# Performance work log

Measured on AMD Instinct MI355X. Metric: run time of the kernel, lower is better.

The kernel has to match this reference:

```python
import jax, jax.numpy as jnp
import numpy as np

P = 0.8
XINT_MAX = 0.125; ROT_MAX = 10.0
BRI_STD = 0.2; CON_STD = 0.2; HUE_MAX = 0.95; SAT_STD = 0.2; SHARP_STD = 1.0; NOISE_STD = 0.1

def _gate(key, B, p):
    k1, k2 = jax.random.split(key)
    bern = jax.random.randint(k1, (B,), 0, 2).astype(jnp.float32)
    u = jax.random.uniform(k2, ())
    return bern * p > u  # [B] bool, matches randint(0,2)*flag*p > random()

def _sel(m, new, old):
    return jnp.where(m[:, None, None, None], new, old)

def _warp(imgs, angle_deg, tx, ty, nearest=False):
    # inverse-affine resample: rotate by angle (deg, CCW) about center, then translate (tx,ty) px; zero fill
    B, C, H, W = imgs.shape
    th = jnp.deg2rad(jnp.asarray(angle_deg, jnp.float32))
    c, s = jnp.cos(th), jnp.sin(th)
    cy, cx = (H - 1) / 2.0, (W - 1) / 2.0
    ys, xs = jnp.meshgrid(jnp.arange(H, dtype=jnp.float32), jnp.arange(W, dtype=jnp.float32), indexing='ij')
    dx = xs - cx - tx; dy = ys - cy - ty
    sx = c * dx + s * dy + cx
    sy = -s * dx + c * dy + cy
    if nearest:
        xi = jnp.round(sx); yi = jnp.round(sy)
        valid = (xi >= 0) & (xi < W) & (yi >= 0) & (yi < H)
        xc = jnp.clip(xi, 0, W - 1).astype(jnp.int32)
        yc = jnp.clip(yi, 0, H - 1).astype(jnp.int32)
        return imgs[:, :, yc, xc] * valid
    x0 = jnp.floor(sx); y0 = jnp.floor(sy)
    wx = sx - x0; wy = sy - y0
    def g(yi, xi):
        valid = (xi >= 0) & (xi < W) & (yi >= 0) & (yi < H)
        yc = jnp.clip(yi, 0, H - 1).astype(jnp.int32)
        xc = jnp.clip(xi, 0, W - 1).astype(jnp.int32)
        return imgs[:, :, yc, xc] * valid
    v00 = g(y0, x0); v01 = g(y0, x0 + 1); v10 = g(y0 + 1, x0); v11 = g(y0 + 1, x0 + 1)
    top = v00 * (1 - wx) + v01 * wx
    bot = v10 * (1 - wx) + v11 * wx
    return top * (1 - wy) + bot * wy

def _gray(x):
    return 0.2989 * x[:, 0:1] + 0.587 * x[:, 1:2] + 0.114 * x[:, 2:3]

def _blend(a, b, ratio):
    return jnp.clip(ratio * a + (1.0 - ratio) * b, 0.0, 1.0)

def _rgb_to_hsv(x):
    r, g, b = x[:, 0], x[:, 1], x[:, 2]
    maxc = jnp.maximum(jnp.maximum(r, g), b)
    minc = jnp.minimum(jnp.minimum(r, g), b)
    cr = maxc - minc
    s = cr / jnp.where(maxc == 0, 1.0, maxc)
    crd = jnp.where(cr == 0, 1.0, cr)
    rc = (maxc - r) / crd; gc = (maxc - g) / crd; bc = (maxc - b) / crd
    h = jnp.where(maxc == r, bc - gc, jnp.where(maxc == g, 2.0 + rc - bc, 4.0 + gc - rc))
    h = jnp.where(cr == 0, 0.0, (h / 6.0) % 1.0)
    return jnp.stack([h, s, maxc], axis=1)

def _hsv_to_rgb(x):
    h, s, v = x[:, 0], x[:, 1], x[:, 2]
    i = jnp.floor(h * 6.0)
    f = h * 6.0 - i
    p = v * (1 - s); q = v * (1 - f * s); t = v * (1 - (1 - f) * s)
    ii = i.astype(jnp.int32) % 6
    conds = [ii == 0, ii == 1, ii == 2, ii == 3, ii == 4, ii == 5]
    r = jnp.select(conds, [v, q, p, p, t, v])
    g = jnp.select(conds, [t, v, v, q, p, p])
    b = jnp.select(conds, [p, p, t, v, v, q])
    return jnp.stack([r, g, b], axis=1)

def _sharp_degenerate(x):
    C, H, W = x.shape[1], x.shape[2], x.shape[3]
    k = jnp.array([[1., 1., 1.], [1., 5., 1.], [1., 1., 1.]], jnp.float32) / 13.0
    w = jnp.tile(k[None, None], (C, 1, 1, 1))
    blur = jax.lax.conv_general_dilated(x, w, (1, 1), 'SAME', feature_group_count=C,
                                        dimension_numbers=('NCHW', 'OIHW', 'NCHW'))
    blur = jnp.clip(blur, 0.0, 1.0)
    interior = jnp.zeros((H, W), bool).at[1:-1, 1:-1].set(True)
    return jnp.where(interior, blur, x)  # torchvision keeps original border pixels

def _augment(images, masks):
    key = jax.random.key(42)
    ks = jax.random.split(key, 18)
    B = images.shape[0]
    img = (images + 1.0) * 0.5
    msk = masks
    # xflip
    m = _gate(ks[0], B, P)
    img = _sel(m, img[:, :, :, ::-1], img)
    msk = _sel(m, msk[:, :, :, ::-1], msk)
    # rotate90 (square images: exact)
    m = _gate(ks[1], B, P)
    img = _sel(m, jnp.rot90(img, 1, axes=(2, 3)), img)
    msk = _sel(m, jnp.rot90(msk, 1, axes=(2, 3)), msk)
    # xint translation
    m = _gate(ks[2], B, P)
    t = jax.random.uniform(ks[3], ()) * XINT_MAX
    img = _sel(m, _warp(img, 0.0, t, t), img)
    msk = _sel(m, _warp(msk, 0.0, t, t, nearest=True), msk)
    # rotate
    m = _gate(ks[4], B, P)
    r = jax.random.uniform(ks[5], ()) * ROT_MAX
    img = _sel(m, _warp(img, r, 0.0, 0.0), img)
    msk = _sel(m, _warp(msk, r, 0.0, 0.0, nearest=True), msk)
    # hue
    m = _gate(ks[6], B, P)
    h = (jax.random.uniform(ks[7], ()) - 0.5) * HUE_MAX
    hsv = _rgb_to_hsv(jnp.clip(img, 0.0, 1.0))
    hsv = hsv.at[:, 0].set((hsv[:, 0] + h) % 1.0)
    img = _sel(m, _hsv_to_rgb(hsv), img)
    # brightness
    m = _gate(ks[8], B, P)
    b = jnp.abs(1.0 + jax.random.normal(ks[9], ()) * BRI_STD)
    img = _sel(m, jnp.clip(img * b, 0.0, 1.0), img)
    # contrast
    m = _gate(ks[10], B, P)
    c = jnp.abs(1.0 + jax.random.normal(ks[11], ()) * CON_STD)
    mean = _gray(img).mean(axis=(2, 3), keepdims=True)
    img = _sel(m, _blend(img, mean, c), img)
    # saturation
    m = _gate(ks[12], B, P)
    s = jnp.abs(1.0 + jax.random.normal(ks[13], ()) * SAT_STD)
    img = _sel(m, _blend(img, _gray(img), s), img)
    # sharpness (bug-faithful: std == self.sharpness == 1.0)
    m = _gate(ks[14], B, P)
    sh = jnp.abs(1.0 + jax.random.normal(ks[15], ()) * SHARP_STD)
    img = _sel(m, _blend(img, _sharp_degenerate(img), sh), img)
    # noise
    m = _gate(ks[16], B, P)
    n = jax.random.normal(ks[17], img.shape, img.dtype) * NOISE_STD
    img = _sel(m, img + n, img)
    img = (img - 0.5) / 0.5
    return img, msk

def setup_inputs() -> dict:
    key = jax.random.key(0)
    k1, k2 = jax.random.split(key)
    images = jax.random.uniform(k1, (32, 3, 512, 512), jnp.float32, -1.0, 1.0)
    masks = (jax.random.uniform(k2, (32, 1, 512, 512), jnp.float32) > 0.5).astype(jnp.float32)
    return {"images": images, "masks": masks}

def reference(images, masks):
    return _augment(images, masks)
```

## Files before the change

kernel.cpp:

```cpp
#include <hip/hip_runtime.h>
#include <stdint.h>
#include <math.h>

#define HH 512
#define WW 512
#define BB 32
#define CC 3
#define HWSZ (HH*WW)
#define CHW (CC*HWSZ)
#define NIMG (BB*CHW)
#define NMSK (BB*HWSZ)

__host__ __device__ inline uint32_t rotl32(uint32_t x, uint32_t r){ return (x<<r)|(x>>(32u-r)); }

__host__ __device__ inline void tf2x32(uint32_t k0, uint32_t k1, uint32_t x0, uint32_t x1,
                                       uint32_t& o0, uint32_t& o1){
  uint32_t kx = k0 ^ k1 ^ 0x1BD11BDAu;
  uint32_t ks[3] = {k0, k1, kx};
  const uint32_t R[2][4] = {{13u,15u,26u,6u},{17u,29u,16u,24u}};
  x0 += ks[0]; x1 += ks[1];
  #pragma unroll
  for (int i = 0; i < 5; ++i){
    #pragma unroll
    for (int j = 0; j < 4; ++j){
      x0 += x1; x1 = rotl32(x1, R[i & 1][j]); x1 ^= x0;
    }
    x0 += ks[(i+1)%3];
    x1 += ks[(i+2)%3] + (uint32_t)(i+1);
  }
  o0 = x0; o1 = x1;
}

__host__ __device__ inline float bits_to_u01(uint32_t b){
  uint32_t fb = (b >> 9) | 0x3f800000u;
  float f;
#ifdef __HIP_DEVICE_COMPILE__
  f = __uint_as_float(fb);
#else
  union { uint32_t u; float f; } cv; cv.u = fb; f = cv.f;
#endif
  return f - 1.0f;
}

__host__ __device__ inline float erfinv_f32(float x){
  float w = -log1pf(-x*x);
  float p;
  if (w < 5.0f){
    w -= 2.5f;
    p = 2.81022636e-08f;
    p = fmaf(p, w, 3.43273939e-07f);
    p = fmaf(p, w, -3.5233877e-06f);
    p = fmaf(p, w, -4.39150654e-06f);
    p = fmaf(p, w, 0.00021858087f);
    p = fmaf(p, w, -0.00125372503f);
    p = fmaf(p, w, -0.00417768164f);
    p = fmaf(p, w, 0.246640727f);
    p = fmaf(p, w, 1.50140941f);
  } else {
    w = sqrtf(w) - 3.0f;
    p = -0.000200214257f;
    p = fmaf(p, w, 0.000100950558f);
    p = fmaf(p, w, 0.00134934322f);
    p = fmaf(p, w, -0.00367342844f);
    p = fmaf(p, w, 0.00573950773f);
    p = fmaf(p, w, -0.0076224613f);
    p = fmaf(p, w, 0.00943887047f);
    p = fmaf(p, w, 1.00167406f);
    p = fmaf(p, w, 2.83297682f);
  }
  return p * x;
}

#define NRM_LO (-0.9999999403953552f)
#define SQRT2F 1.41421356237309504880f

__host__ __device__ inline float normal_from_bits(uint32_t b){
  float f = bits_to_u01(b);
  float val = f * 2.0f + NRM_LO;
  val = fmaxf(NRM_LO, val);
  return SQRT2F * erfinv_f32(val);
}

struct Key { uint32_t a, b; };

static Key foldSplit(Key k, uint32_t j){
  Key r; tf2x32(k.a, k.b, 0u, j, r.a, r.b); return r;
}

static uint32_t bits32(Key k, uint32_t i){
  uint32_t o0, o1; tf2x32(k.a, k.b, 0u, i, o0, o1); return o0 ^ o1;
}

static float unif_scalar(Key k){ return bits_to_u01(bits32(k, 0u)); }
static float normal_scalar(Key k){ return normal_from_bits(bits32(k, 0u)); }

static uint32_t gate_mask(Key kg){
  Key k1 = foldSplit(kg, 0u);
  Key k2 = foldSplit(kg, 1u);
  Key kl = foldSplit(k1, 1u);
  float u = bits_to_u01(bits32(k2, 0u));
  uint32_t m = 0;
  for (uint32_t i = 0; i < 32; ++i){
    float bern = (float)(bits32(kl, i) & 1u);
    if (bern * 0.8f > u) m |= (1u << i);
  }
  return m;
}

struct AugParams {
  uint32_t mFlip, mRot90, mTrans, mRot, mHue, mBri, mCon, mSat, mSharp, mNoise;
  float t, rotC, rotS, hShift, bri, con, sat, shp;
  uint32_t nk0, nk1;
};

__device__ inline float clip01(float v){ return fminf(fmaxf(v, 0.0f), 1.0f); }

__device__ inline void permIdx(int y, int x, bool r9, bool fl, int& py, int& px){
  if (r9){ py = x; px = 511 - y; } else { py = y; px = x; }
  if (fl) px = 511 - px;
}

__device__ inline float tapP(const float* __restrict__ src, int y, int x, bool r9, bool fl){
  if ((unsigned)x >= 512u || (unsigned)y >= 512u) return 0.0f;
  int py, px; permIdx(y, x, r9, fl, py, px);
  return (src[py*512 + px] + 1.0f) * 0.5f;
}

__device__ inline void stage1RGB(const float* __restrict__ base, int ty, int tx,
                                 bool r9, bool fl, bool tr, float t, float out[3]){
  if (!tr){
    #pragma unroll
    for (int c = 0; c < 3; ++c) out[c] = tapP(base + c*HWSZ, ty, tx, r9, fl);
    return;
  }
  float sx = (((float)tx - 255.5f) - t) + 255.5f;
  float sy = (((float)ty - 255.5f) - t) + 255.5f;
  float x0f = floorf(sx), y0f = floorf(sy);
  float wx = sx - x0f, wy = sy - y0f;
  int x0 = (int)x0f, y0 = (int)y0f;
  #pragma unroll
  for (int c = 0; c < 3; ++c){
    const float* s = base + c*HWSZ;
    float v00 = tapP(s, y0,   x0,   r9, fl);
    float v01 = tapP(s, y0,   x0+1, r9, fl);
    float v10 = tapP(s, y0+1, x0,   r9, fl);
    float v11 = tapP(s, y0+1, x0+1, r9, fl);
    float top = v00*(1.0f-wx) + v01*wx;
    float bot = v10*(1.0f-wx) + v11*wx;
    out[c] = top*(1.0f-wy) + bot*wy;
  }
}

__device__ inline void rotTap(const float* __restrict__ base, int ty, int tx,
                              bool r9, bool fl, bool tr, float t, float o[3]){
  if ((unsigned)tx < 512u && (unsigned)ty < 512u){
    stage1RGB(base, ty, tx, r9, fl, tr, t, o);
  } else {
    o[0] = o[1] = o[2] = 0.0f;
  }
}

__device__ inline void rgb2hsv(float r, float g, float b, float& h, float& s, float& v){
  float maxc = fmaxf(fmaxf(r, g), b);
  float minc = fminf(fminf(r, g), b);
  float cr = maxc - minc;
  s = cr / ((maxc == 0.0f) ? 1.0f : maxc);
  float crd = (cr == 0.0f) ? 1.0f : cr;
  float rc = (maxc - r) / crd;
  float gc = (maxc - g) / crd;
  float bc = (maxc - b) / crd;
  float hh;
  if (maxc == r)      hh = bc - gc;
  else if (maxc == g) hh = 2.0f + rc - bc;
  else                hh = 4.0f + gc - rc;
  if (cr == 0.0f) hh = 0.0f;
  else { hh = hh / 6.0f; hh = hh - floorf(hh); }
  h = hh; v = maxc;
}

__device__ inline void hsv2rgb(float h, float s, float v, float& r, float& g, float& b){
  float i = floorf(h * 6.0f);
  float f = h * 6.0f - i;
  float p = v * (1.0f - s);
  float q = v * (1.0f - f * s);
  float t = v * (1.0f - (1.0f - f) * s);
  int ii = ((int)i) % 6;
  switch (ii){
    case 0: r = v; g = t; b = p; break;
    case 1: r = q; g = v; b = p; break;
    case 2: r = p; g = v; b = t; break;
    case 3: r = p; g = q; b = v; break;
    case 4: r = t; g = p; b = v; break;
    default: r = v; g = p; b = q; break;
  }
}

__device__ inline void applyHB(float v[3], bool hue, bool bri, const AugParams& P){
  if (hue){
    float r = clip01(v[0]), g = clip01(v[1]), bb = clip01(v[2]);
    float h, s, val;
    rgb2hsv(r, g, bb, h, s, val);
    h = h + P.hShift;
    h = h - floorf(h);
    hsv2rgb(h, s, val, v[0], v[1], v[2]);
  }
  if (bri){
    #pragma unroll
    for (int c = 0; c < 3; ++c) v[c] = clip01(v[c] * P.bri);
  }
}

__device__ inline void stage2RGB(const float* __restrict__ base, int yy, int xx,
                                 const AugParams& P, int b, float v[3]){
  bool fl  = (P.mFlip  >> b) & 1u;
  bool r9  = (P.mRot90 >> b) & 1u;
  bool tr  = (P.mTrans >> b) & 1u;
  bool rot = (P.mRot   >> b) & 1u;
  if (rot){
    float dx = (float)xx - 255.5f;
    float dy = (float)yy - 255.5f;
    float sx = (P.rotC*dx + P.rotS*dy) + 255.5f;
    float sy = (-P.rotS*dx + P.rotC*dy) + 255.5f;
    float x0f = floorf(sx), y0f = floorf(sy);
    float wx = sx - x0f, wy = sy - y0f;
    int x0 = (int)x0f, y0 = (int)y0f;
    float q00[3], q01[3], q10[3], q11[3];
    rotTap(base, y0,   x0,   r9, fl, tr, P.t, q00);
    rotTap(base, y0,   x0+1, r9, fl, tr, P.t, q01);
    rotTap(base, y0+1, x0,   r9, fl, tr, P.t, q10);
    rotTap(base, y0+1, x0+1, r9, fl, tr, P.t, q11);
    #pragma unroll
    for (int c = 0; c < 3; ++c){
      float top = q00[c]*(1.0f-wx) + q01[c]*wx;
      float bot = q10[c]*(1.0f-wx) + q11[c]*wx;
      v[c] = top*(1.0f-wy) + bot*wy;
    }
  } else {
    stage1RGB(base, yy, xx, r9, fl, tr, P.t, v);
  }
  applyHB(v, (P.mHue >> b) & 1u, (P.mBri >> b) & 1u, P);
}

__device__ inline float s1at(const float* __restrict__ s, int y, int x){
  return ((unsigned)x < 512u && (unsigned)y < 512u) ? s[y*512 + x] : 0.0f;
}

__device__ inline void stage2S1(const float* __restrict__ s1b, int yy, int xx,
                                const AugParams& P, int b, float v[3]){
  bool rot = (P.mRot >> b) & 1u;
  bool hue = (P.mHue >> b) & 1u;
  bool bri = (P.mBri >> b) & 1u;
  if (rot){
    float dx = (float)xx - 255.5f;
    float dy = (float)yy - 255.5f;
    float sx = (P.rotC*dx + P.rotS*dy) + 255.5f;
    float sy = (-P.rotS*dx + P.rotC*dy) + 255.5f;
    float x0f = floorf(sx), y0f = floorf(sy);
    float wx = sx - x0f, wy = sy - y0f;
    int x0 = (int)x0f, y0 = (int)y0f;
    #pragma unroll
    for (int c = 0; c < 3; ++c){
      const float* s = s1b + c*HWSZ;
      float v00 = s1at(s, y0,   x0);
      float v01 = s1at(s, y0,   x0+1);
      float v10 = s1at(s, y0+1, x0);
      float v11 = s1at(s, y0+1, x0+1);
      float top = v00*(1.0f-wx) + v01*wx;
      float bot = v10*(1.0f-wx) + v11*wx;
      v[c] = top*(1.0f-wy) + bot*wy;
    }
  } else {
    #pragma unroll
    for (int c = 0; c < 3; ++c) v[c] = s1b[c*HWSZ + yy*512 + xx];
  }
  applyHB(v, hue, bri, P);
}

__device__ inline void procCS(float v[3], bool con, float cmul, float cadd, bool sat, float smul){
  if (con){
    #pragma unroll
    for (int c = 0; c < 3; ++c) v[c] = clip01(cmul * v[c] + cadd);
  }
  if (sat){
    float g = 0.2989f*v[0] + 0.587f*v[1] + 0.114f*v[2];
    float gadd = (1.0f - smul) * g;
    #pragma unroll
    for (int c = 0; c < 3; ++c) v[c] = clip01(smul * v[c] + gadd);
  }
}


__global__ void kZero(float* meanAcc){
  int t = threadIdx.x;
  if (t < 32) meanAcc[t] = 0.0f;
}


__global__ __launch_bounds__(256) void kStage1(const float* __restrict__ img,
                                               float* __restrict__ S1, AugParams P){
  __shared__ float ptile[33][33];
  int b = blockIdx.z;
  bool fl = (P.mFlip  >> b) & 1u;
  bool r9 = (P.mRot90 >> b) & 1u;
  bool tr = (P.mTrans >> b) & 1u;
  int X0 = blockIdx.x*32, Y0 = blockIdx.y*32;
  int tx = threadIdx.x, ty = threadIdx.y;
  int tid = ty*32 + tx;
  const float* base = img + (size_t)b*CHW;
  float t = P.t;

  if (!r9 && !tr){
    #pragma unroll
    for (int c = 0; c < 3; ++c){
      const float* src = base + c*HWSZ;
      float* dst = S1 + (size_t)b*CHW + (size_t)c*HWSZ;
      #pragma unroll
      for (int k = 0; k < 4; ++k){
        int y = Y0 + ty + 8*k;
        int x = X0 + tx;
        int px = fl ? (511 - x) : x;
        dst[(size_t)y*512 + x] = (src[y*512 + px] + 1.0f) * 0.5f;
      }
    }
    return;
  }

  for (int c = 0; c < 3; ++c){
    const float* src = base + c*HWSZ;
    for (int idx = tid; idx < 33*33; idx += 256){
      int r = idx / 33, q = idx - r*33;
      float val = 0.0f;
      if (!r9){
        int yy = Y0 - 1 + r;
        int xx = X0 - 1 + q;
        if ((unsigned)yy < 512u && (unsigned)xx < 512u){
          int px = fl ? (511 - xx) : xx;
          val = (src[yy*512 + px] + 1.0f) * 0.5f;
        }
        ptile[r][q] = val;
      } else {
        int xx = X0 - 1 + r;
        int yy = Y0 - 1 + q;
        if ((unsigned)yy < 512u && (unsigned)xx < 512u){
          int col = fl ? yy : (511 - yy);
          val = (src[xx*512 + col] + 1.0f) * 0.5f;
        }
        ptile[q][r] = val;
      }
    }
    __syncthreads();
    #pragma unroll
    for (int k = 0; k < 4; ++k){
      int y = Y0 + ty + 8*k;
      int x = X0 + tx;
      float o;
      if (tr){
        float sx = (((float)x - 255.5f) - t) + 255.5f;
        float sy = (((float)y - 255.5f) - t) + 255.5f;
        float x0f = floorf(sx), y0f = floorf(sy);
        float wx = sx - x0f, wy = sy - y0f;
        int lx0 = (int)x0f - (X0 - 1);
        int ly0 = (int)y0f - (Y0 - 1);
        float v00 = ptile[ly0][lx0],     v01 = ptile[ly0][lx0+1];
        float v10 = ptile[ly0+1][lx0],   v11 = ptile[ly0+1][lx0+1];
        float top = v00*(1.0f-wx) + v01*wx;
        float bot = v10*(1.0f-wx) + v11*wx;
        o = top*(1.0f-wy) + bot*wy;
      } else {
        o = ptile[ty + 8*k + 1][tx + 1];
      }
      S1[(size_t)b*CHW + (size_t)c*HWSZ + (size_t)y*512 + x] = o;
    }
    __syncthreads();
  }
}

__global__ __launch_bounds__(256) void kMaskStage(const float* __restrict__ msk,
                                                  float* __restrict__ M1,
                                                  float* __restrict__ outMsk, AugParams P){
  __shared__ float mtile[32][33];
  int b = blockIdx.z;
  bool fl  = (P.mFlip  >> b) & 1u;
  bool r9  = (P.mRot90 >> b) & 1u;
  bool rot = (P.mRot   >> b) & 1u;
  int X0 = blockIdx.x*32, Y0 = blockIdx.y*32;
  int tx = threadIdx.x, ty = threadIdx.y;
  int tid = ty*32 + tx;
  const float* src = msk + (size_t)b*HWSZ;
  float* dst = (rot ? M1 : outMsk) + (size_t)b*HWSZ;
  if (!r9){
    #pragma unroll
    for (int k = 0; k < 4; ++k){
      int y = Y0 + ty + 8*k, x = X0 + tx;
      int px = fl ? (511 - x) : x;
      dst[y*512 + x] = src[y*512 + px];
    }
  } else {
    for (int idx = tid; idx < 32*32; idx += 256){
      int r = idx >> 5, q = idx & 31;
      int xx = X0 + r;
      int yy = Y0 + q;
      int col = fl ? yy : (511 - yy);
      mtile[q][r] = src[xx*512 + col];
    }
    __syncthreads();
    #pragma unroll
    for (int k = 0; k < 4; ++k){
      int y = Y0 + ty + 8*k, x = X0 + tx;
      dst[y*512 + x] = mtile[ty + 8*k][tx];
    }
  }
}

__global__ __launch_bounds__(256) void kMaskRot(const float* __restrict__ M1,
                                                float* __restrict__ outMsk, AugParams P){
  int b = blockIdx.z;
  if (!((P.mRot >> b) & 1u)) return;
  int x = blockIdx.x*blockDim.x + threadIdx.x;
  int y = blockIdx.y*blockDim.y + threadIdx.y;
  float dx = __fsub_rn((float)x, 255.5f);
  float dy = __fsub_rn((float)y, 255.5f);
  float sx = __fadd_rn(__fadd_rn(__fmul_rn(P.rotC, dx), __fmul_rn(P.rotS, dy)), 255.5f);
  float sy = __fadd_rn(__fadd_rn(__fmul_rn(-P.rotS, dx), __fmul_rn(P.rotC, dy)), 255.5f);
  float xi = rintf(sx), yi = rintf(sy);
  bool valid = (xi >= 0.0f) && (xi < 512.0f) && (yi >= 0.0f) && (yi < 512.0f);
  int xc = (int)fminf(fmaxf(xi, 0.0f), 511.0f);
  int yc = (int)fminf(fmaxf(yi, 0.0f), 511.0f);
  float v = valid ? M1[(size_t)b*HWSZ + yc*512 + xc] : 0.0f;
  outMsk[(size_t)b*HWSZ + y*512 + x] = v;
}

__global__ __launch_bounds__(256) void kMean2(const float* __restrict__ S1,
                                              float* __restrict__ meanAcc, AugParams P){
  int b = blockIdx.z;
  if (!((P.mCon >> b) & 1u)) return;
  bool rot = (P.mRot >> b) & 1u;
  bool hue = (P.mHue >> b) & 1u;
  bool bri = (P.mBri >> b) & 1u;
  int tid = threadIdx.x;
  const float* base = S1 + (size_t)b*CHW;
  int pbase = blockIdx.x * 4096;
  float lsum = 0.0f;

  if (!rot){
    const float4* r4p = (const float4*)(base);
    const float4* g4p = (const float4*)(base + HWSZ);
    const float4* b4p = (const float4*)(base + 2*HWSZ);
    int q0 = (pbase >> 2) + tid;
    #pragma unroll
    for (int j = 0; j < 4; ++j){
      float4 r4 = r4p[q0 + j*256];
      float4 g4 = g4p[q0 + j*256];
      float4 b4 = b4p[q0 + j*256];
      float rr[4] = {r4.x, r4.y, r4.z, r4.w};
      float gg[4] = {g4.x, g4.y, g4.z, g4.w};
      float bb[4] = {b4.x, b4.y, b4.z, b4.w};
      #pragma unroll
      for (int e = 0; e < 4; ++e){
        float v[3] = {rr[e], gg[e], bb[e]};
        applyHB(v, hue, bri, P);
        lsum += 0.2989f*v[0] + 0.587f*v[1] + 0.114f*v[2];
      }
    }
  } else {
    #pragma unroll 4
    for (int j = 0; j < 16; ++j){
      int px = pbase + j*256 + tid;
      int y = px >> 9, x = px & 511;
      float v[3];
      stage2S1(base, y, x, P, b, v);
      lsum += 0.2989f*v[0] + 0.587f*v[1] + 0.114f*v[2];
    }
  }

  #pragma unroll
  for (int off = 32; off > 0; off >>= 1) lsum += __shfl_down(lsum, off);
  __shared__ float wsum[4];
  int wid = tid >> 6, lid = tid & 63;
  if (lid == 0) wsum[wid] = lsum;
  __syncthreads();
  if (tid == 0) atomicAdd(&meanAcc[b], wsum[0] + wsum[1] + wsum[2] + wsum[3]);
}

__global__ __launch_bounds__(256) void kFinal2(const float* __restrict__ S1,
                                               const float* __restrict__ meanAcc,
                                               float* __restrict__ out, AugParams P){
  __shared__ float s2[34][34][3];
  int tx = threadIdx.x, ty = threadIdx.y;
  int tid = ty*32 + tx;
  int bx = blockIdx.x, by = blockIdx.y, b = blockIdx.z;
  const float W1 = 1.0f/13.0f, W5 = 5.0f/13.0f;

  bool con = (P.mCon   >> b) & 1u;
  bool sat = (P.mSat   >> b) & 1u;
  bool shg = (P.mSharp >> b) & 1u;
  bool noi = (P.mNoise >> b) & 1u;
  float mean = meanAcc[b] * (1.0f/262144.0f);
  float cadd = (1.0f - P.con) * mean;
  const float* base = S1 + (size_t)b*CHW;

  for (int cell = tid; cell < 34*34; cell += 256){
    int r = cell / 34, cc = cell - r*34;
    int gy = by*32 + r - 1, gx = bx*32 + cc - 1;
    float v[3] = {0.0f, 0.0f, 0.0f};
    if ((unsigned)gx < 512u && (unsigned)gy < 512u){
      stage2S1(base, gy, gx, P, b, v);
      procCS(v, con, P.con, cadd, sat, P.sat);
    }
    s2[r][cc][0] = v[0]; s2[r][cc][1] = v[1]; s2[r][cc][2] = v[2];
  }
  __syncthreads();

  for (int k = 0; k < 4; ++k){
    int yy = ty + 8*k;
    int x = bx*32 + tx, y = by*32 + yy;
    bool interior = (x >= 1) && (x <= 510) && (y >= 1) && (y <= 510);
    float res[3];
    float c0[3] = { s2[yy+1][tx+1][0], s2[yy+1][tx+1][1], s2[yy+1][tx+1][2] };
    if (shg && interior){
      float nsum[3] = {0.0f, 0.0f, 0.0f};
      #pragma unroll
      for (int dy = 0; dy < 3; ++dy){
        #pragma unroll
        for (int dxx = 0; dxx < 3; ++dxx){
          if (dxx == 1 && dy == 1) continue;
          #pragma unroll
          for (int c = 0; c < 3; ++c) nsum[c] += s2[yy+dy][tx+dxx][c];
        }
      }
      #pragma unroll
      for (int c = 0; c < 3; ++c){
        float bl = clip01(nsum[c]*W1 + c0[c]*W5);
        res[c] = clip01(P.shp * c0[c] + (1.0f - P.shp) * bl);
      }
    } else {
      res[0] = c0[0]; res[1] = c0[1]; res[2] = c0[2];
    }

    if (noi){
      #pragma unroll
      for (int c = 0; c < 3; ++c){
        uint32_t idx = (uint32_t)(b*CHW + c*HWSZ + y*512 + x);
        uint32_t o0, o1;
        tf2x32(P.nk0, P.nk1, 0u, idx, o0, o1);
        res[c] += normal_from_bits(o0 ^ o1) * 0.1f;
      }
    }
    #pragma unroll
    for (int c = 0; c < 3; ++c){
      out[(size_t)b*CHW + (size_t)c*HWSZ + (size_t)y*512 + x] = (res[c] - 0.5f) * 2.0f;
    }
  }
}


__global__ __launch_bounds__(256) void kMask(const float* __restrict__ msk,
                                             float* __restrict__ out, AugParams P){
  int x = blockIdx.x*blockDim.x + threadIdx.x;
  int y = blockIdx.y*blockDim.y + threadIdx.y;
  int b = blockIdx.z;
  bool fl  = (P.mFlip  >> b) & 1u;
  bool r9  = (P.mRot90 >> b) & 1u;
  bool rot = (P.mRot   >> b) & 1u;
  float v;
  if (rot){
    float dx = __fsub_rn((float)x, 255.5f);
    float dy = __fsub_rn((float)y, 255.5f);
    float sx = __fadd_rn(__fadd_rn(__fmul_rn(P.rotC, dx), __fmul_rn(P.rotS, dy)), 255.5f);
    float sy = __fadd_rn(__fadd_rn(__fmul_rn(-P.rotS, dx), __fmul_rn(P.rotC, dy)), 255.5f);
    float xi = rintf(sx), yi = rintf(sy);
    bool valid = (xi >= 0.0f) && (xi < 512.0f) && (yi >= 0.0f) && (yi < 512.0f);
    int xc = (int)fminf(fmaxf(xi, 0.0f), 511.0f);
    int yc = (int)fminf(fmaxf(yi, 0.0f), 511.0f);
    int py, px; permIdx(yc, xc, r9, fl, py, px);
    v = valid ? msk[(size_t)b*HWSZ + py*512 + px] : 0.0f;
  } else {
    int py, px; permIdx(y, x, r9, fl, py, px);
    v = msk[(size_t)b*HWSZ + py*512 + px];
  }
  out[(size_t)b*HWSZ + y*512 + x] = v;
}

__global__ __launch_bounds__(256) void kMean(const float* __restrict__ img,
                                             float* __restrict__ meanAcc, AugParams P){
  int b = blockIdx.z;
  if (!((P.mCon >> b) & 1u)) return;
  int x = blockIdx.x*blockDim.x + threadIdx.x;
  int y = blockIdx.y*blockDim.y + threadIdx.y;
  float v[3];
  stage2RGB(img + (size_t)b*CHW, y, x, P, b, v);
  float gray = 0.2989f*v[0] + 0.587f*v[1] + 0.114f*v[2];
  __shared__ float sred[256];
  int tid = threadIdx.y*blockDim.x + threadIdx.x;
  sred[tid] = gray;
  __syncthreads();
  for (int s = 128; s > 0; s >>= 1){
    if (tid < s) sred[tid] += sred[tid + s];
    __syncthreads();
  }
  if (tid == 0) atomicAdd(&meanAcc[b], sred[0]);
}

__global__ __launch_bounds__(256) void kFinal(const float* __restrict__ img,
                                              const float* __restrict__ meanAcc,
                                              float* __restrict__ out, AugParams P){
  __shared__ float s2[10][34][3];
  int tx = threadIdx.x, ty = threadIdx.y;
  int tid = ty*32 + tx;
  int bx = blockIdx.x, by = blockIdx.y, b = blockIdx.z;
  const float W1 = 1.0f/13.0f, W5 = 5.0f/13.0f;

  bool con = (P.mCon   >> b) & 1u;
  bool sat = (P.mSat   >> b) & 1u;
  bool shg = (P.mSharp >> b) & 1u;
  bool noi = (P.mNoise >> b) & 1u;
  float mean = meanAcc[b] * (1.0f/262144.0f);
  float cadd = (1.0f - P.con) * mean;
  const float* base = img + (size_t)b*CHW;

  for (int cell = tid; cell < 340; cell += 256){
    int r = cell / 34, cc = cell % 34;
    int gy = by*8 + r - 1, gx = bx*32 + cc - 1;
    float v[3] = {0.0f, 0.0f, 0.0f};
    if ((unsigned)gx < 512u && (unsigned)gy < 512u){
      stage2RGB(base, gy, gx, P, b, v);
      procCS(v, con, P.con, cadd, sat, P.sat);
    }
    s2[r][cc][0] = v[0]; s2[r][cc][1] = v[1]; s2[r][cc][2] = v[2];
  }
  __syncthreads();

  int x = bx*32 + tx, y = by*8 + ty;
  bool interior = (x >= 1) && (x <= 510) && (y >= 1) && (y <= 510);
  float res[3];
  float c0[3] = { s2[ty+1][tx+1][0], s2[ty+1][tx+1][1], s2[ty+1][tx+1][2] };
  if (shg && interior){
    float nsum[3] = {0.0f, 0.0f, 0.0f};
    #pragma unroll
    for (int dy = 0; dy < 3; ++dy){
      #pragma unroll
      for (int dxx = 0; dxx < 3; ++dxx){
        if (dxx == 1 && dy == 1) continue;
        #pragma unroll
        for (int c = 0; c < 3; ++c) nsum[c] += s2[ty+dy][tx+dxx][c];
      }
    }
    #pragma unroll
    for (int c = 0; c < 3; ++c){
      float bl = clip01(nsum[c]*W1 + c0[c]*W5);
      res[c] = clip01(P.shp * c0[c] + (1.0f - P.shp) * bl);
    }
  } else {
    res[0] = c0[0]; res[1] = c0[1]; res[2] = c0[2];
  }

  if (noi){
    #pragma unroll
    for (int c = 0; c < 3; ++c){
      uint32_t idx = (uint32_t)(b*CHW + c*HWSZ + y*512 + x);
      uint32_t o0, o1;
      tf2x32(P.nk0, P.nk1, 0u, idx, o0, o1);
      res[c] += normal_from_bits(o0 ^ o1) * 0.1f;
    }
  }
  #pragma unroll
  for (int c = 0; c < 3; ++c){
    out[(size_t)b*CHW + (size_t)c*HWSZ + y*512 + x] = (res[c] - 0.5f) * 2.0f;
  }
}

extern "C" void kernel_launch(void* const* d_in, const int* in_sizes, int n_in,
                              void* d_out, int out_size, void* d_ws, size_t ws_size,
                              hipStream_t stream) {
  (void)in_sizes; (void)n_in; (void)out_size;
  const float* images = (const float*)d_in[0];
  const float* masks  = (const float*)d_in[1];
  float* out_img = (float*)d_out;
  float* out_msk = out_img + (size_t)NIMG;
  float* meanAcc = (float*)d_ws;

  Key root; root.a = 0u; root.b = 42u;
  Key ks[18];
  for (uint32_t j = 0; j < 18; ++j) ks[j] = foldSplit(root, j);

  AugParams P;
  P.mFlip  = gate_mask(ks[0]);
  P.mRot90 = gate_mask(ks[1]);
  P.mTrans = gate_mask(ks[2]);
  P.t      = unif_scalar(ks[3]) * 0.125f;
  P.mRot   = gate_mask(ks[4]);
  float r  = unif_scalar(ks[5]) * 10.0f;
  P.mHue   = gate_mask(ks[6]);
  P.hShift = (unif_scalar(ks[7]) - 0.5f) * 0.95f;
  P.mBri   = gate_mask(ks[8]);
  P.bri    = fabsf(1.0f + normal_scalar(ks[9])  * 0.2f);
  P.mCon   = gate_mask(ks[10]);
  P.con    = fabsf(1.0f + normal_scalar(ks[11]) * 0.2f);
  P.mSat   = gate_mask(ks[12]);
  P.sat    = fabsf(1.0f + normal_scalar(ks[13]) * 0.2f);
  P.mSharp = gate_mask(ks[14]);
  P.shp    = fabsf(1.0f + normal_scalar(ks[15]) * 1.0f);
  P.mNoise = gate_mask(ks[16]);
  P.nk0 = ks[17].a; P.nk1 = ks[17].b;

  if (!(P.t > 0.0f)) P.mTrans = 0u;

  float th = r * 0.017453292519943295f;
  P.rotC = (float)cos((double)th);
  P.rotS = (float)sin((double)th);

  dim3 blk(32, 8, 1);
  const size_t needFull = ((size_t)NIMG + (size_t)NMSK + 64) * sizeof(float);
  const size_t needImg  = ((size_t)NIMG + 64) * sizeof(float);

  kZero<<<1, 64, 0, stream>>>(meanAcc);

  if (ws_size >= needFull){
    float* S1 = (float*)d_ws + 64;
    float* M1 = S1 + (size_t)NIMG;
    kMaskStage<<<dim3(16, 16, 32), blk, 0, stream>>>(masks, M1, out_msk, P);
    kMaskRot  <<<dim3(16, 64, 32), blk, 0, stream>>>(M1, out_msk, P);
    kStage1   <<<dim3(16, 16, 32), blk, 0, stream>>>(images, S1, P);
    kMean2    <<<dim3(64, 1, 32), dim3(256,1,1), 0, stream>>>(S1, meanAcc, P);
    kFinal2   <<<dim3(16, 16, 32), blk, 0, stream>>>(S1, meanAcc, out_img, P);
  } else if (ws_size >= needImg){
    float* S1 = (float*)d_ws + 64;
    kMask     <<<dim3(16, 64, 32), blk, 0, stream>>>(masks, out_msk, P);
    kStage1   <<<dim3(16, 16, 32), blk, 0, stream>>>(images, S1, P);
    kMean2    <<<dim3(64, 1, 32), dim3(256,1,1), 0, stream>>>(S1, meanAcc, P);
    kFinal2   <<<dim3(16, 16, 32), blk, 0, stream>>>(S1, meanAcc, out_img, P);
  } else {
    kMask <<<dim3(16, 64, 32), blk, 0, stream>>>(masks, out_msk, P);
    kMean <<<dim3(16, 64, 32), blk, 0, stream>>>(images, meanAcc, P);
    kFinal<<<dim3(16, 64, 32), blk, 0, stream>>>(images, meanAcc, out_img, P);
  }
}
```

Baseline: 378.6 us.

## Fuse contrast mean into stage1 and add no-sharpen fast path in final

For non-rotated images, the gray mean that contrast needs is now accumulated inside kStage1 while the pixels are written, so kMean2 only rereads S1 for rotated images. kStage1 gets separate paths for translate-only (a direct stage1RGB call) and rot90 (a tile holding all three channels). kFinal2 gets a path that skips the shared-memory halo tile when sharpening is off, and kMaskRot now has each thread handle four rows with a smaller grid. This removes a full reread of the image workspace and some shared-memory staging, at the cost of more registers and atomics in stage1.

```diff
diff --git a/kernel.cpp b/kernel.cpp
--- a/kernel.cpp
+++ b/kernel.cpp
@@ -297,63 +297,80 @@
 
 
 __global__ __launch_bounds__(256) void kStage1(const float* __restrict__ img,
-                                               float* __restrict__ S1, AugParams P){
-  __shared__ float ptile[33][33];
+                                               float* __restrict__ S1,
+                                               float* __restrict__ meanAcc, AugParams P){
+  __shared__ float ptile[3][33][33];
+  __shared__ float wsum[4];
   int b = blockIdx.z;
-  bool fl = (P.mFlip  >> b) & 1u;
-  bool r9 = (P.mRot90 >> b) & 1u;
-  bool tr = (P.mTrans >> b) & 1u;
+  bool fl  = (P.mFlip  >> b) & 1u;
+  bool r9  = (P.mRot90 >> b) & 1u;
+  bool tr  = (P.mTrans >> b) & 1u;
+  bool rot = (P.mRot   >> b) & 1u;
+  bool con = (P.mCon   >> b) & 1u;
+  bool hue = (P.mHue   >> b) & 1u;
+  bool bri = (P.mBri   >> b) & 1u;
+  bool accM = con && !rot;
   int X0 = blockIdx.x*32, Y0 = blockIdx.y*32;
   int tx = threadIdx.x, ty = threadIdx.y;
   int tid = ty*32 + tx;
   const float* base = img + (size_t)b*CHW;
+  float* dstb = S1 + (size_t)b*CHW;
   float t = P.t;
+  float gsum = 0.0f;
 
   if (!r9 && !tr){
+    #pragma unroll
+    for (int k = 0; k < 4; ++k){
+      int y = Y0 + ty + 8*k, x = X0 + tx;
+      int px = fl ? (511 - x) : x;
+      float v[3];
+      #pragma unroll
+      for (int c = 0; c < 3; ++c){
+        v[c] = (base[c*HWSZ + y*512 + px] + 1.0f) * 0.5f;
+        dstb[(size_t)c*HWSZ + (size_t)y*512 + x] = v[c];
+      }
+      if (accM){
+        float w[3] = {v[0], v[1], v[2]};
+        applyHB(w, hue, bri, P);
+        gsum += 0.2989f*w[0] + 0.587f*w[1] + 0.114f*w[2];
+      }
+    }
+  } else if (!r9){
+    #pragma unroll
+    for (int k = 0; k < 4; ++k){
+      int y = Y0 + ty + 8*k, x = X0 + tx;
+      float v[3];
+      stage1RGB(base, y, x, false, fl, true, t, v);
+      #pragma unroll
+      for (int c = 0; c < 3; ++c)
+        dstb[(size_t)c*HWSZ + (size_t)y*512 + x] = v[c];
+      if (accM){
+        float w[3] = {v[0], v[1], v[2]};
+        applyHB(w, hue, bri, P);
+        gsum += 0.2989f*w[0] + 0.587f*w[1] + 0.114f*w[2];
+      }
+    }
+  } else {
     #pragma unroll
     for (int c = 0; c < 3; ++c){
       const float* src = base + c*HWSZ;
-      float* dst = S1 + (size_t)b*CHW + (size_t)c*HWSZ;
-      #pragma unroll
-      for (int k = 0; k < 4; ++k){
-        int y = Y0 + ty + 8*k;
-        int x = X0 + tx;
-        int px = fl ? (511 - x) : x;
-        dst[(size_t)y*512 + x] = (src[y*512 + px] + 1.0f) * 0.5f;
-      }
-    }
-    return;
-  }
-
-  for (int c = 0; c < 3; ++c){
-    const float* src = base + c*HWSZ;
-    for (int idx = tid; idx < 33*33; idx += 256){
-      int r = idx / 33, q = idx - r*33;
-      float val = 0.0f;
-      if (!r9){
-        int yy = Y0 - 1 + r;
-        int xx = X0 - 1 + q;
-        if ((unsigned)yy < 512u && (unsigned)xx < 512u){
-          int px = fl ? (511 - xx) : xx;
-          val = (src[yy*512 + px] + 1.0f) * 0.5f;
-        }
-        ptile[r][q] = val;
-      } else {
+      for (int idx = tid; idx < 33*33; idx += 256){
+        int r = idx / 33, q = idx - r*33;
         int xx = X0 - 1 + r;
         int yy = Y0 - 1 + q;
+        float val = 0.0f;
         if ((unsigned)yy < 512u && (unsigned)xx < 512u){
           int col = fl ? yy : (511 - yy);
           val = (src[xx*512 + col] + 1.0f) * 0.5f;
         }
-        ptile[q][r] = val;
+        ptile[c][q][r] = val;
       }
     }
     __syncthreads();
     #pragma unroll
     for (int k = 0; k < 4; ++k){
-      int y = Y0 + ty + 8*k;
-      int x = X0 + tx;
-      float o;
+      int y = Y0 + ty + 8*k, x = X0 + tx;
+      float v[3];
       if (tr){
         float sx = (((float)x - 255.5f) - t) + 255.5f;
         float sy = (((float)y - 255.5f) - t) + 255.5f;
@@ -361,17 +378,36 @@
         float wx = sx - x0f, wy = sy - y0f;
         int lx0 = (int)x0f - (X0 - 1);
         int ly0 = (int)y0f - (Y0 - 1);
-        float v00 = ptile[ly0][lx0],     v01 = ptile[ly0][lx0+1];
-        float v10 = ptile[ly0+1][lx0],   v11 = ptile[ly0+1][lx0+1];
-        float top = v00*(1.0f-wx) + v01*wx;
-        float bot = v10*(1.0f-wx) + v11*wx;
-        o = top*(1.0f-wy) + bot*wy;
+        #pragma unroll
+        for (int c = 0; c < 3; ++c){
+          float v00 = ptile[c][ly0][lx0],   v01 = ptile[c][ly0][lx0+1];
+          float v10 = ptile[c][ly0+1][lx0], v11 = ptile[c][ly0+1][lx0+1];
+          float top = v00*(1.0f-wx) + v01*wx;
+          float bot = v10*(1.0f-wx) + v11*wx;
+          v[c] = top*(1.0f-wy) + bot*wy;
+        }
       } else {
-        o = ptile[ty + 8*k + 1][tx + 1];
-      }
-      S1[(size_t)b*CHW + (size_t)c*HWSZ + (size_t)y*512 + x] = o;
-    }
+        #pragma unroll
+        for (int c = 0; c < 3; ++c) v[c] = ptile[c][ty+8*k+1][tx+1];
+      }
+      #pragma unroll
+      for (int c = 0; c < 3; ++c)
+        dstb[(size_t)c*HWSZ + (size_t)y*512 + x] = v[c];
+      if (accM){
+        float w[3] = {v[0], v[1], v[2]};
+        applyHB(w, hue, bri, P);
+        gsum += 0.2989f*w[0] + 0.587f*w[1] + 0.114f*w[2];
+      }
+    }
+  }
+
+  if (accM){
+    #pragma unroll
+    for (int off = 32; off > 0; off >>= 1) gsum += __shfl_down(gsum, off);
+    int wid = tid >> 6, lid = tid & 63;
+    if (lid == 0) wsum[wid] = gsum;
     __syncthreads();
+    if (tid == 0) atomicAdd(&meanAcc[b], wsum[0] + wsum[1] + wsum[2] + wsum[3]);
   }
 }
 
@@ -416,61 +452,42 @@
                                                 float* __restrict__ outMsk, AugParams P){
   int b = blockIdx.z;
   if (!((P.mRot >> b) & 1u)) return;
-  int x = blockIdx.x*blockDim.x + threadIdx.x;
-  int y = blockIdx.y*blockDim.y + threadIdx.y;
-  float dx = __fsub_rn((float)x, 255.5f);
-  float dy = __fsub_rn((float)y, 255.5f);
-  float sx = __fadd_rn(__fadd_rn(__fmul_rn(P.rotC, dx), __fmul_rn(P.rotS, dy)), 255.5f);
-  float sy = __fadd_rn(__fadd_rn(__fmul_rn(-P.rotS, dx), __fmul_rn(P.rotC, dy)), 255.5f);
-  float xi = rintf(sx), yi = rintf(sy);
-  bool valid = (xi >= 0.0f) && (xi < 512.0f) && (yi >= 0.0f) && (yi < 512.0f);
-  int xc = (int)fminf(fmaxf(xi, 0.0f), 511.0f);
-  int yc = (int)fminf(fmaxf(yi, 0.0f), 511.0f);
-  float v = valid ? M1[(size_t)b*HWSZ + yc*512 + xc] : 0.0f;
-  outMsk[(size_t)b*HWSZ + y*512 + x] = v;
+  int X0 = blockIdx.x*32, Y0 = blockIdx.y*32;
+  int tx = threadIdx.x, ty = threadIdx.y;
+  const float* src = M1 + (size_t)b*HWSZ;
+  float* dst = outMsk + (size_t)b*HWSZ;
+  #pragma unroll
+  for (int k = 0; k < 4; ++k){
+    int x = X0 + tx, y = Y0 + ty + 8*k;
+    float dx = __fsub_rn((float)x, 255.5f);
+    float dy = __fsub_rn((float)y, 255.5f);
+    float sx = __fadd_rn(__fadd_rn(__fmul_rn(P.rotC, dx), __fmul_rn(P.rotS, dy)), 255.5f);
+    float sy = __fadd_rn(__fadd_rn(__fmul_rn(-P.rotS, dx), __fmul_rn(P.rotC, dy)), 255.5f);
+    float xi = rintf(sx), yi = rintf(sy);
+    bool valid = (xi >= 0.0f) && (xi < 512.0f) && (yi >= 0.0f) && (yi < 512.0f);
+    int xc = (int)fminf(fmaxf(xi, 0.0f), 511.0f);
+    int yc = (int)fminf(fmaxf(yi, 0.0f), 511.0f);
+    float v = valid ? src[yc*512 + xc] : 0.0f;
+    dst[y*512 + x] = v;
+  }
 }
 
 __global__ __launch_bounds__(256) void kMean2(const float* __restrict__ S1,
                                               float* __restrict__ meanAcc, AugParams P){
   int b = blockIdx.z;
-  if (!((P.mCon >> b) & 1u)) return;
-  bool rot = (P.mRot >> b) & 1u;
-  bool hue = (P.mHue >> b) & 1u;
-  bool bri = (P.mBri >> b) & 1u;
+  if (!((P.mCon >> b) & 1u) || !((P.mRot >> b) & 1u)) return;
   int tid = threadIdx.x;
   const float* base = S1 + (size_t)b*CHW;
   int pbase = blockIdx.x * 4096;
   float lsum = 0.0f;
 
-  if (!rot){
-    const float4* r4p = (const float4*)(base);
-    const float4* g4p = (const float4*)(base + HWSZ);
-    const float4* b4p = (const float4*)(base + 2*HWSZ);
-    int q0 = (pbase >> 2) + tid;
-    #pragma unroll
-    for (int j = 0; j < 4; ++j){
-      float4 r4 = r4p[q0 + j*256];
-      float4 g4 = g4p[q0 + j*256];
-      float4 b4 = b4p[q0 + j*256];
-      float rr[4] = {r4.x, r4.y, r4.z, r4.w};
-      float gg[4] = {g4.x, g4.y, g4.z, g4.w};
-      float bb[4] = {b4.x, b4.y, b4.z, b4.w};
-      #pragma unroll
-      for (int e = 0; e < 4; ++e){
-        float v[3] = {rr[e], gg[e], bb[e]};
-        applyHB(v, hue, bri, P);
-        lsum += 0.2989f*v[0] + 0.587f*v[1] + 0.114f*v[2];
-      }
-    }
-  } else {
-    #pragma unroll 4
-    for (int j = 0; j < 16; ++j){
-      int px = pbase + j*256 + tid;
-      int y = px >> 9, x = px & 511;
-      float v[3];
-      stage2S1(base, y, x, P, b, v);
-      lsum += 0.2989f*v[0] + 0.587f*v[1] + 0.114f*v[2];
-    }
+  #pragma unroll 4
+  for (int j = 0; j < 16; ++j){
+    int px = pbase + j*256 + tid;
+    int y = px >> 9, x = px & 511;
+    float v[3];
+    stage2S1(base, y, x, P, b, v);
+    lsum += 0.2989f*v[0] + 0.587f*v[1] + 0.114f*v[2];
   }
 
   #pragma unroll
@@ -499,6 +516,30 @@
   float cadd = (1.0f - P.con) * mean;
   const float* base = S1 + (size_t)b*CHW;
 
+  if (!shg){
+    #pragma unroll
+    for (int k = 0; k < 4; ++k){
+      int x = bx*32 + tx, y = by*32 + ty + 8*k;
+      float res[3];
+      stage2S1(base, y, x, P, b, res);
+      procCS(res, con, P.con, cadd, sat, P.sat);
+      if (noi){
+        #pragma unroll
+        for (int c = 0; c < 3; ++c){
+          uint32_t idx = (uint32_t)(b*CHW + c*HWSZ + y*512 + x);
+          uint32_t o0, o1;
+          tf2x32(P.nk0, P.nk1, 0u, idx, o0, o1);
+          res[c] += normal_from_bits(o0 ^ o1) * 0.1f;
+        }
+      }
+      #pragma unroll
+      for (int c = 0; c < 3; ++c){
+        out[(size_t)b*CHW + (size_t)c*HWSZ + (size_t)y*512 + x] = (res[c] - 0.5f) * 2.0f;
+      }
+    }
+    return;
+  }
+
   for (int cell = tid; cell < 34*34; cell += 256){
     int r = cell / 34, cc = cell - r*34;
     int gy = by*32 + r - 1, gx = bx*32 + cc - 1;
@@ -517,7 +558,7 @@
     bool interior = (x >= 1) && (x <= 510) && (y >= 1) && (y <= 510);
     float res[3];
     float c0[3] = { s2[yy+1][tx+1][0], s2[yy+1][tx+1][1], s2[yy+1][tx+1][2] };
-    if (shg && interior){
+    if (interior){
       float nsum[3] = {0.0f, 0.0f, 0.0f};
       #pragma unroll
       for (int dy = 0; dy < 3; ++dy){
@@ -719,14 +760,14 @@
     float* S1 = (float*)d_ws + 64;
     float* M1 = S1 + (size_t)NIMG;
     kMaskStage<<<dim3(16, 16, 32), blk, 0, stream>>>(masks, M1, out_msk, P);
-    kMaskRot  <<<dim3(16, 64, 32), blk, 0, stream>>>(M1, out_msk, P);
-    kStage1   <<<dim3(16, 16, 32), blk, 0, stream>>>(images, S1, P);
+    kMaskRot  <<<dim3(16, 16, 32), blk, 0, stream>>>(M1, out_msk, P);
+    kStage1   <<<dim3(16, 16, 32), blk, 0, stream>>>(images, S1, meanAcc, P);
     kMean2    <<<dim3(64, 1, 32), dim3(256,1,1), 0, stream>>>(S1, meanAcc, P);
     kFinal2   <<<dim3(16, 16, 32), blk, 0, stream>>>(S1, meanAcc, out_img, P);
   } else if (ws_size >= needImg){
     float* S1 = (float*)d_ws + 64;
     kMask     <<<dim3(16, 64, 32), blk, 0, stream>>>(masks, out_msk, P);
-    kStage1   <<<dim3(16, 16, 32), blk, 0, stream>>>(images, S1, P);
+    kStage1   <<<dim3(16, 16, 32), blk, 0, stream>>>(images, S1, meanAcc, P);
     kMean2    <<<dim3(64, 1, 32), dim3(256,1,1), 0, stream>>>(S1, meanAcc, P);
     kFinal2   <<<dim3(16, 16, 32), blk, 0, stream>>>(S1, meanAcc, out_img, P);
   } else {
```

Measured after the change: 374.6 us. No clear change (-1.0%).
